# Performance work log

Measured on AMD Instinct MI355X. Metric: run time of the kernel, lower is better.

Reference implementation:

```python
import jax, jax.numpy as jnp
import numpy as np
from jax import lax

B, C, L = 8, 256, 2048
DK, DV, KS = 256, 256, 3
PAD = (KS - 1) // 2  # odd kernel -> dilation 1, same-length padding


def conv1d(x, w, b):
    # x: (B, C, L), w: (O, C, KS), b: (O,)
    y = lax.conv_general_dilated(
        x, w, window_strides=(1,), padding=[(PAD, PAD)],
        rhs_dilation=(1,), dimension_numbers=("NCH", "OIH", "NCH"))
    return y + b[None, :, None]


def setup_inputs() -> dict:
    key = jax.random.key(0)
    ks = jax.random.split(key, 7)
    sc = 1.0 / np.sqrt(C * KS)
    return {
        "x": jax.random.normal(ks[0], (B, C, L), dtype=jnp.float32),
        "Wq": jax.random.normal(ks[1], (DK, C, KS), dtype=jnp.float32) * sc,
        "bq": jnp.zeros((DK,), dtype=jnp.float32),
        "Wk": jax.random.normal(ks[2], (DK, C, KS), dtype=jnp.float32) * sc,
        "bk": jnp.zeros((DK,), dtype=jnp.float32),
        "Wv": jax.random.normal(ks[3], (DV, C, KS), dtype=jnp.float32) * sc,
        "bv": jnp.zeros((DV,), dtype=jnp.float32),
    }


def reference(x, Wq, bq, Wk, bk, Wv, bv):
    Q = conv1d(x, Wq, bq)  # (B, DK, L)
    K = conv1d(x, Wk, bk)  # (B, DK, L)
    V = conv1d(x, Wv, bv)  # (B, DV, L)
    # A = softmax(Q^T K / sqrt(dk)) over key axis
    scores = jnp.einsum("bdq,bdk->bqk", Q, K) / jnp.sqrt(jnp.float32(DK))
    A = jax.nn.softmax(scores, axis=2)  # (B, L, L)
    H = jnp.einsum("bqk,bdk->bdq", A, V)  # (B, DV, L)
    return H
```

## Files before the change

kernel.cpp:

```cpp
#include <hip/hip_runtime.h>
#include <hip/hip_bf16.h>
#include <stdint.h>


typedef __bf16 bf16;
typedef __bf16 bf16x2 __attribute__((ext_vector_type(2)));
typedef __bf16 bf16x4 __attribute__((ext_vector_type(4)));
typedef __bf16 bf16x8 __attribute__((ext_vector_type(8)));
typedef float f32x4 __attribute__((ext_vector_type(4)));
typedef uint32_t u32x4 __attribute__((ext_vector_type(4)));
typedef __attribute__((address_space(1))) const uint32_t cu32_as1;
typedef __attribute__((address_space(3))) uint32_t u32_as3;

#define DEVI __device__ __forceinline__
#define LOG2E 1.44269504088896f

DEVI void async_copy16(const void* g, void* l) {
  __builtin_amdgcn_global_load_lds((cu32_as1*)g, (u32_as3*)l, 16, 0, 0);
}

DEVI void block_sync() {
  asm volatile("" ::: "memory");
  __builtin_amdgcn_sched_barrier(0);
  __builtin_amdgcn_s_barrier();
  __builtin_amdgcn_sched_barrier(0);
  asm volatile("" ::: "memory");
}

#define VMCNT(n) asm volatile("s_waitcnt vmcnt(" #n ")" ::: "memory")

__global__ void prep_w(const float* __restrict__ Wq, const float* __restrict__ Wk,
                       const float* __restrict__ Wv, const float* __restrict__ bq,
                       const float* __restrict__ bk, const float* __restrict__ bv,
                       bf16* __restrict__ W2, float* __restrict__ biasA) {
  const float QSC = 0.0625f * LOG2E;
  int idx = blockIdx.x * 256 + threadIdx.x;
  if (idx < 768 * 768) {
    int o = idx / 768, kk = idx - o * 768;
    int ks = kk >> 8, c = kk & 255;
    const float* W = (o < 256) ? Wq : ((o < 512) ? Wk : Wv);
    int ol = o & 255;
    float w = W[ol * 768 + c * 3 + ks];
    if (o < 256) w *= QSC;
    W2[o * 768 + kk] = (bf16)w;
  }
  if (idx < 768) {
    float v;
    if (idx < 256) v = bq[idx] * QSC;
    else if (idx < 512) v = bk[idx - 256];
    else v = bv[idx - 512];
    biasA[idx] = v;
  }
}

__global__ void prep_x(const float* __restrict__ x, bf16* __restrict__ xT) {
  __shared__ float tile[32][33];
  int bid = blockIdx.x;
  int lt = bid & 63, ct = (bid >> 6) & 7, b = bid >> 9;
  int t = threadIdx.x;
  int tl = t & 31, tc = t >> 5;
  const float* xb = x + (size_t)b * 256 * 2048;
#pragma unroll
  for (int i = 0; i < 4; ++i) {
    int c = ct * 32 + tc + i * 8;
    tile[tc + i * 8][tl] = xb[(size_t)c * 2048 + lt * 32 + tl];
  }
  __syncthreads();
  bf16* xTb = xT + (size_t)b * 2050 * 256;
#pragma unroll
  for (int i = 0; i < 4; ++i) {
    int l = lt * 32 + tc + i * 8;
    xTb[(size_t)(l + 1) * 256 + ct * 32 + tl] = (bf16)tile[tl][tc + i * 8];
  }
  if (lt == 0 && t < 32) xTb[ct * 32 + t] = (bf16)0.f;
  if (lt == 63 && t < 32) xTb[(size_t)2049 * 256 + ct * 32 + t] = (bf16)0.f;
}

__launch_bounds__(256, 2)
__global__ void conv_gemm(const bf16* __restrict__ W2, const bf16* __restrict__ xT,
                          const float* __restrict__ biasA, bf16* __restrict__ QT,
                          bf16* __restrict__ KT, bf16* __restrict__ V) {
  __shared__ bf16 Alds[128 * 64];
  __shared__ bf16 Blds[128 * 64];
  const int t = threadIdx.x;
  const int w = t >> 6, lane = t & 63;
  const int g = lane >> 4, lr = lane & 15;
  const int wr = w >> 1, wc = w & 1;
  const int bid = blockIdx.x;
  const int b = bid & 7;
  const int rest = bid >> 3;
  const int ot = rest % 6;
  const int lt = rest / 6;
  const int l0 = lt * 128;

  const bf16* xTb = xT + (size_t)b * 2050 * 256;
  const bf16* Ab = W2 + (size_t)(ot * 128) * 768;

  const int srow = t >> 3;
  const int scb = ((t & 7) * 16) ^ ((srow & 7) << 4);

  f32x4 acc[4][4];
#pragma unroll
  for (int i = 0; i < 4; ++i)
#pragma unroll
    for (int j = 0; j < 4; ++j) acc[i][j] = (f32x4){0.f, 0.f, 0.f, 0.f};

  for (int step = 0; step < 12; ++step) {
    const int kk = step * 64;
    const int ks = kk >> 8;
    const int c0 = kk & 255;
    const bf16* As = Ab + kk + (scb >> 1);
    const bf16* Bs = xTb + (size_t)(l0 + ks) * 256 + c0 + (scb >> 1);
#pragma unroll
    for (int i = 0; i < 4; ++i) {
      const int row = srow + i * 32;
      async_copy16(As + (size_t)row * 768, (char*)Alds + w * 1024 + i * 4096);
      async_copy16(Bs + (size_t)row * 256, (char*)Blds + w * 1024 + i * 4096);
    }
    asm volatile("s_waitcnt vmcnt(0)" ::: "memory");
    __syncthreads();
#pragma unroll
    for (int sub = 0; sub < 2; ++sub) {
      bf16x8 af[4], bfr[4];
#pragma unroll
      for (int mf = 0; mf < 4; ++mf) {
        const int row = wr * 64 + mf * 16 + lr;
        const int cb = (sub * 64 + g * 16) ^ ((row & 7) << 4);
        af[mf] = *(const bf16x8*)((const char*)Alds + row * 128 + cb);
      }
#pragma unroll
      for (int nf = 0; nf < 4; ++nf) {
        const int row = wc * 64 + nf * 16 + lr;
        const int cb = (sub * 64 + g * 16) ^ ((row & 7) << 4);
        bfr[nf] = *(const bf16x8*)((const char*)Blds + row * 128 + cb);
      }
#pragma unroll
      for (int mf = 0; mf < 4; ++mf)
#pragma unroll
        for (int nf = 0; nf < 4; ++nf)
          acc[mf][nf] = __builtin_amdgcn_mfma_f32_16x16x32_bf16(af[mf], bfr[nf], acc[mf][nf], 0, 0, 0);
    }
    __syncthreads();
  }

  const int obase = ot * 128 + wr * 64;
  const int lbase = l0 + wc * 64;
  if (ot < 4) {
    bf16* dst = ((ot < 2) ? QT : KT) + (size_t)b * 2048 * 256;
#pragma unroll
    for (int mf = 0; mf < 4; ++mf) {
      const int og = obase + mf * 16 + g * 4;
      float bb[4];
#pragma unroll
      for (int r = 0; r < 4; ++r) bb[r] = biasA[og + r];
#pragma unroll
      for (int nf = 0; nf < 4; ++nf) {
        const int l = lbase + nf * 16 + lr;
        bf16x4 pk;
#pragma unroll
        for (int r = 0; r < 4; ++r) pk[r] = (bf16)(acc[mf][nf][r] + bb[r]);
        *(bf16x4*)(dst + (size_t)l * 256 + (og & 255)) = pk;
      }
    }
  } else {
    bf16* dst = V + (size_t)b * 256 * 2048;
#pragma unroll
    for (int mf = 0; mf < 4; ++mf) {
      const int og = obase + mf * 16 + g * 4;
      float bb[4];
#pragma unroll
      for (int r = 0; r < 4; ++r) bb[r] = biasA[og + r];
      const int ov = og - 512;
#pragma unroll
      for (int nf = 0; nf < 4; ++nf) {
        const int l = lbase + nf * 16 + lr;
#pragma unroll
        for (int r = 0; r < 4; ++r)
          dst[(size_t)(ov + r) * 2048 + l] = (bf16)(acc[mf][nf][r] + bb[r]);
      }
    }
  }
}

__launch_bounds__(256, 2)
__global__ void attn(const bf16* __restrict__ QT, const bf16* __restrict__ KT,
                     const bf16* __restrict__ V, bf16* __restrict__ Opart,
                     float* __restrict__ Sl) {
  __shared__ bf16 Klds[2 * 32 * 256];
  __shared__ bf16 Vlds[2 * 128 * 64];
  const int t = threadIdx.x;
  const int w = t >> 6, lane = t & 63;
  const int g = lane >> 4, lr = lane & 15;
  const int bid = blockIdx.x;
  const int b = bid & 7;
  const int kvh = (bid >> 3) & 3;
  const int qt = bid >> 5;
  const int q0w = qt * 128 + w * 32;
  const int kb0 = kvh * 512;
  const bf16* QTb = QT + (size_t)b * 2048 * 256;
  const bf16* KTb = KT + (size_t)b * 2048 * 256;
  const bf16* Vb = V + (size_t)b * 256 * 2048;

  auto stageK = [&](int kt, int p) {
#pragma unroll
    for (int i = 0; i < 4; ++i) {
      const int row = i * 8 + (t >> 5);
      const int col = ((t & 31) ^ row) * 8;
      const bf16* src = KTb + (size_t)(kb0 + kt * 32 + row) * 256 + col;
      async_copy16(src, (char*)Klds + p * 16384 + i * 4096 + t * 16);
    }
  };
  auto stageV = [&](int kt, int p) {
#pragma unroll
    for (int i = 0; i < 4; ++i) {
      const int row = i * 32 + (t >> 3);
      const int ls = (t & 7) ^ (row & 7);
      const int d = row * 2 + (ls >> 2);
      const int k0 = (ls & 3) * 8;
      const bf16* src = Vb + (size_t)d * 2048 + kb0 + kt * 32 + k0;
      async_copy16(src, (char*)Vlds + p * 16384 + i * 4096 + t * 16);
    }
  };

  bf16x8 qreg[2][8];
#pragma unroll
  for (int qfr = 0; qfr < 2; ++qfr)
#pragma unroll
    for (int ds = 0; ds < 8; ++ds)
      qreg[qfr][ds] = *(const bf16x8*)(QTb + (size_t)(q0w + qfr * 16 + lr) * 256 + ds * 32 + g * 8);

  f32x4 oacc[16][2];
#pragma unroll
  for (int i = 0; i < 16; ++i) {
    oacc[i][0] = (f32x4){0.f, 0.f, 0.f, 0.f};
    oacc[i][1] = (f32x4){0.f, 0.f, 0.f, 0.f};
  }
  float l_acc[2] = {0.f, 0.f};

  stageK(0, 0); stageV(0, 0);
  stageK(1, 1); stageV(1, 1);

  for (int kt = 0; kt < 16; ++kt) {
    const int p = kt & 1;
    if (kt == 15) { VMCNT(0); } else { VMCNT(8); }
    block_sync();

    f32x4 sT[2][2];
#pragma unroll
    for (int kfr = 0; kfr < 2; ++kfr)
#pragma unroll
      for (int qfr = 0; qfr < 2; ++qfr) sT[kfr][qfr] = (f32x4){0.f, 0.f, 0.f, 0.f};
    __builtin_amdgcn_s_setprio(1);
#pragma unroll
    for (int ds = 0; ds < 8; ++ds) {
      bf16x8 kf[2];
#pragma unroll
      for (int kfr = 0; kfr < 2; ++kfr) {
        const int row = kfr * 16 + lr;
        kf[kfr] = *(const bf16x8*)((const char*)Klds + p * 16384 + row * 512 +
                                   (((ds * 4 + g) ^ row) * 16));
      }
#pragma unroll
      for (int kfr = 0; kfr < 2; ++kfr)
#pragma unroll
        for (int qfr = 0; qfr < 2; ++qfr)
          sT[kfr][qfr] = __builtin_amdgcn_mfma_f32_16x16x32_bf16(kf[kfr], qreg[qfr][ds], sT[kfr][qfr], 0, 0, 0);
    }
    __builtin_amdgcn_s_setprio(0);

#pragma unroll
    for (int kfr = 0; kfr < 2; ++kfr)
#pragma unroll
      for (int qfr = 0; qfr < 2; ++qfr)
#pragma unroll
        for (int r = 0; r < 4; ++r) {
          float pe = __builtin_exp2f(sT[kfr][qfr][r]);
          sT[kfr][qfr][r] = pe;
          l_acc[qfr] += pe;
        }

    bf16x8 pB[2];
#pragma unroll
    for (int qfr = 0; qfr < 2; ++qfr) {
      uint32_t wq[2][2];
#pragma unroll
      for (int kfr = 0; kfr < 2; ++kfr)
#pragma unroll
        for (int pp = 0; pp < 2; ++pp) {
          bf16x2 pr;
          pr[0] = (bf16)sT[kfr][qfr][2 * pp];
          pr[1] = (bf16)sT[kfr][qfr][2 * pp + 1];
          wq[kfr][pp] = __builtin_bit_cast(uint32_t, pr);
        }
      uint32_t bw[4];
#pragma unroll
      for (int j = 0; j < 4; ++j) {
        const int srcLane = ((g & 1) * 2 + (j >> 1)) * 16 + lr;
        const uint32_t a = (uint32_t)__shfl((int)wq[0][j & 1], srcLane, 64);
        const uint32_t bb = (uint32_t)__shfl((int)wq[1][j & 1], srcLane, 64);
        bw[j] = (lane < 32) ? a : bb;
      }
      u32x4 v4 = {bw[0], bw[1], bw[2], bw[3]};
      pB[qfr] = __builtin_bit_cast(bf16x8, v4);
    }

    __builtin_amdgcn_s_setprio(1);
#pragma unroll
    for (int dfr = 0; dfr < 16; ++dfr) {
      const int row = dfr * 8 + (lr >> 1);
      bf16x8 vf = *(const bf16x8*)((const char*)Vlds + p * 16384 + row * 128 +
                                   ((((lr & 1) * 4 + g) ^ ((lr >> 1) & 7)) * 16));
      oacc[dfr][0] = __builtin_amdgcn_mfma_f32_16x16x32_bf16(vf, pB[0], oacc[dfr][0], 0, 0, 0);
      oacc[dfr][1] = __builtin_amdgcn_mfma_f32_16x16x32_bf16(vf, pB[1], oacc[dfr][1], 0, 0, 0);
    }
    __builtin_amdgcn_s_setprio(0);
    block_sync();
    if (kt < 14) { stageK(kt + 2, p); stageV(kt + 2, p); }
  }

#pragma unroll
  for (int qfr = 0; qfr < 2; ++qfr) {
    float rv = l_acc[qfr];
    rv += __shfl_xor(rv, 16, 64);
    rv += __shfl_xor(rv, 32, 64);
    l_acc[qfr] = rv;
  }

  bf16* Op = Opart + (size_t)bid * 128 * 256;
#pragma unroll
  for (int qfr = 0; qfr < 2; ++qfr) {
    const int ql = w * 32 + qfr * 16 + lr;
#pragma unroll
    for (int dfr = 0; dfr < 16; ++dfr) {
      const int d0 = dfr * 16 + g * 4;
      bf16x4 pk;
#pragma unroll
      for (int r = 0; r < 4; ++r) pk[r] = (bf16)oacc[dfr][qfr][r];
      *(bf16x4*)(Op + (size_t)ql * 256 + d0) = pk;
    }
    if (g == 0) Sl[bid * 128 + ql] = l_acc[qfr];
  }
}

__launch_bounds__(256)
__global__ void merge_p(const bf16* __restrict__ Opart, const float* __restrict__ Sl,
                        float* __restrict__ H) {
  __shared__ float Ocomb[32][257];
  const int bid = blockIdx.x;
  const int b = bid & 7;
  const int qt = (bid >> 3) & 15;
  const int qc = bid >> 7;
  const int t = threadIdx.x;
  float* Hb = H + (size_t)b * 256 * 2048 + qt * 128 + qc * 32;

  for (int qq = 0; qq < 32; ++qq) {
    const int ql = qc * 32 + qq;
    float wsum = 0.f, o = 0.f;
#pragma unroll
    for (int kvh = 0; kvh < 4; ++kvh) {
      const int blk = b + 8 * kvh + 32 * qt;
      wsum += Sl[blk * 128 + ql];
      o += (float)Opart[((size_t)blk * 128 + ql) * 256 + t];
    }
    Ocomb[qq][t] = o / wsum;
  }
  __syncthreads();
  const int q = t & 31;
  const int dbase = (t >> 5) * 32;
#pragma unroll
  for (int j = 0; j < 32; ++j) {
    const int d = dbase + j;
    Hb[(size_t)d * 2048 + q] = Ocomb[q][d];
  }
}

extern "C" void kernel_launch(void* const* d_in, const int* in_sizes, int n_in,
                              void* d_out, int out_size, void* d_ws, size_t ws_size,
                              hipStream_t stream) {
  (void)in_sizes; (void)n_in; (void)out_size; (void)ws_size;
  const float* x = (const float*)d_in[0];
  const float* Wq = (const float*)d_in[1];
  const float* bq = (const float*)d_in[2];
  const float* Wk = (const float*)d_in[3];
  const float* bk = (const float*)d_in[4];
  const float* Wv = (const float*)d_in[5];
  const float* bv = (const float*)d_in[6];
  char* ws = (char*)d_ws;
  bf16* xT = (bf16*)(ws + 0);
  bf16* W2 = (bf16*)(ws + 8396800);
  float* biasA = (float*)(ws + 9576448);
  bf16* QT = (bf16*)(ws + 9580544);
  bf16* KT = (bf16*)(ws + 17969152);
  bf16* V = (bf16*)(ws + 26357760);
  bf16* Opart = (bf16*)(ws + 34746368);
  float* Sl = (float*)(ws + 68300800);
  float* H = (float*)d_out;

  prep_w<<<dim3(2304), dim3(256), 0, stream>>>(Wq, Wk, Wv, bq, bk, bv, W2, biasA);
  prep_x<<<dim3(4096), dim3(256), 0, stream>>>(x, xT);
  conv_gemm<<<dim3(768), dim3(256), 0, stream>>>(W2, xT, biasA, QT, KT, V);
  attn<<<dim3(512), dim3(256), 0, stream>>>(QT, KT, V, Opart, Sl);
  merge_p<<<dim3(512), dim3(256), 0, stream>>>(Opart, Sl, H);
}
```

Before: 113.3 us.

## Share softmax probabilities via LDS and split the PV product across waves by head dim

Each wave now writes its exponentiated score tile as bf16 into a new shared LDS buffer. The PV matmul is repartitioned so that every wave covers all 128 queries but only a quarter of the value dimension, replacing the cross-lane shuffle packing of P. This cuts per-wave V fragment reads from LDS. The load pipeline is also reordered: V is staged one tile ahead right after the top barrier, and K two tiles ahead after the P barrier. The cost is an extra block barrier per iteration, an LDS write/read round-trip for P, and an lgkmcnt(0) wait added to every barrier.

```diff
diff --git a/kernel.cpp b/kernel.cpp
--- a/kernel.cpp
+++ b/kernel.cpp
@@ -22,6 +22,7 @@
 DEVI void block_sync() {
   asm volatile("" ::: "memory");
   __builtin_amdgcn_sched_barrier(0);
+  asm volatile("s_waitcnt lgkmcnt(0)" ::: "memory");
   __builtin_amdgcn_s_barrier();
   __builtin_amdgcn_sched_barrier(0);
   asm volatile("" ::: "memory");
@@ -188,6 +189,7 @@
                      float* __restrict__ Sl) {
   __shared__ bf16 Klds[2 * 32 * 256];
   __shared__ bf16 Vlds[2 * 128 * 64];
+  __shared__ bf16 Plds[64 * 64];
   const int t = threadIdx.x;
   const int w = t >> 6, lane = t & 63;
   const int g = lane >> 4, lr = lane & 15;
@@ -224,32 +226,33 @@
 
   bf16x8 qreg[2][8];
 #pragma unroll
-  for (int qfr = 0; qfr < 2; ++qfr)
+  for (int qf = 0; qf < 2; ++qf)
 #pragma unroll
     for (int ds = 0; ds < 8; ++ds)
-      qreg[qfr][ds] = *(const bf16x8*)(QTb + (size_t)(q0w + qfr * 16 + lr) * 256 + ds * 32 + g * 8);
-
-  f32x4 oacc[16][2];
-#pragma unroll
-  for (int i = 0; i < 16; ++i) {
-    oacc[i][0] = (f32x4){0.f, 0.f, 0.f, 0.f};
-    oacc[i][1] = (f32x4){0.f, 0.f, 0.f, 0.f};
-  }
+      qreg[qf][ds] = *(const bf16x8*)(QTb + (size_t)(q0w + qf * 16 + lr) * 256 + ds * 32 + g * 8);
+
+  f32x4 oacc[4][8];
+#pragma unroll
+  for (int i = 0; i < 4; ++i)
+#pragma unroll
+    for (int j = 0; j < 8; ++j) oacc[i][j] = (f32x4){0.f, 0.f, 0.f, 0.f};
   float l_acc[2] = {0.f, 0.f};
 
-  stageK(0, 0); stageV(0, 0);
-  stageK(1, 1); stageV(1, 1);
+  stageK(0, 0);
+  stageV(0, 0);
+  stageK(1, 1);
 
   for (int kt = 0; kt < 16; ++kt) {
     const int p = kt & 1;
-    if (kt == 15) { VMCNT(0); } else { VMCNT(8); }
+    if (kt == 15) { VMCNT(0); } else { VMCNT(4); }
     block_sync();
+    if (kt < 15) stageV(kt + 1, p ^ 1);
 
     f32x4 sT[2][2];
 #pragma unroll
     for (int kfr = 0; kfr < 2; ++kfr)
 #pragma unroll
-      for (int qfr = 0; qfr < 2; ++qfr) sT[kfr][qfr] = (f32x4){0.f, 0.f, 0.f, 0.f};
+      for (int qf = 0; qf < 2; ++qf) sT[kfr][qf] = (f32x4){0.f, 0.f, 0.f, 0.f};
     __builtin_amdgcn_s_setprio(1);
 #pragma unroll
     for (int ds = 0; ds < 8; ++ds) {
@@ -263,82 +266,71 @@
 #pragma unroll
       for (int kfr = 0; kfr < 2; ++kfr)
 #pragma unroll
-        for (int qfr = 0; qfr < 2; ++qfr)
-          sT[kfr][qfr] = __builtin_amdgcn_mfma_f32_16x16x32_bf16(kf[kfr], qreg[qfr][ds], sT[kfr][qfr], 0, 0, 0);
+        for (int qf = 0; qf < 2; ++qf)
+          sT[kfr][qf] = __builtin_amdgcn_mfma_f32_16x16x32_bf16(kf[kfr], qreg[qf][ds], sT[kfr][qf], 0, 0, 0);
     }
     __builtin_amdgcn_s_setprio(0);
 
 #pragma unroll
     for (int kfr = 0; kfr < 2; ++kfr)
 #pragma unroll
-      for (int qfr = 0; qfr < 2; ++qfr)
+      for (int qf = 0; qf < 2; ++qf) {
+        bf16x4 pk;
 #pragma unroll
         for (int r = 0; r < 4; ++r) {
-          float pe = __builtin_exp2f(sT[kfr][qfr][r]);
-          sT[kfr][qfr][r] = pe;
-          l_acc[qfr] += pe;
+          float pe = __builtin_exp2f(sT[kfr][qf][r]);
+          l_acc[qf] += pe;
+          pk[r] = (bf16)pe;
         }
-
-    bf16x8 pB[2];
-#pragma unroll
-    for (int qfr = 0; qfr < 2; ++qfr) {
-      uint32_t wq[2][2];
-#pragma unroll
-      for (int kfr = 0; kfr < 2; ++kfr)
-#pragma unroll
-        for (int pp = 0; pp < 2; ++pp) {
-          bf16x2 pr;
-          pr[0] = (bf16)sT[kfr][qfr][2 * pp];
-          pr[1] = (bf16)sT[kfr][qfr][2 * pp + 1];
-          wq[kfr][pp] = __builtin_bit_cast(uint32_t, pr);
-        }
-      uint32_t bw[4];
-#pragma unroll
-      for (int j = 0; j < 4; ++j) {
-        const int srcLane = ((g & 1) * 2 + (j >> 1)) * 16 + lr;
-        const uint32_t a = (uint32_t)__shfl((int)wq[0][j & 1], srcLane, 64);
-        const uint32_t bb = (uint32_t)__shfl((int)wq[1][j & 1], srcLane, 64);
-        bw[j] = (lane < 32) ? a : bb;
-      }
-      u32x4 v4 = {bw[0], bw[1], bw[2], bw[3]};
-      pB[qfr] = __builtin_bit_cast(bf16x8, v4);
-    }
+        const int q = w * 32 + qf * 16 + lr;
+        const int row = q >> 1;
+        const int slot = (lr & 1) * 4 + kfr * 2 + (g >> 1);
+        const int byte = row * 128 + ((slot ^ (row & 7)) << 4) + (g & 1) * 8;
+        *(bf16x4*)((char*)Plds + byte) = pk;
+      }
+    block_sync();
+    if (kt < 14) stageK(kt + 2, p);
 
     __builtin_amdgcn_s_setprio(1);
-#pragma unroll
-    for (int dfr = 0; dfr < 16; ++dfr) {
-      const int row = dfr * 8 + (lr >> 1);
-      bf16x8 vf = *(const bf16x8*)((const char*)Vlds + p * 16384 + row * 128 +
-                                   ((((lr & 1) * 4 + g) ^ ((lr >> 1) & 7)) * 16));
-      oacc[dfr][0] = __builtin_amdgcn_mfma_f32_16x16x32_bf16(vf, pB[0], oacc[dfr][0], 0, 0, 0);
-      oacc[dfr][1] = __builtin_amdgcn_mfma_f32_16x16x32_bf16(vf, pB[1], oacc[dfr][1], 0, 0, 0);
+    bf16x8 pB[8];
+#pragma unroll
+    for (int qfr = 0; qfr < 8; ++qfr) {
+      const int row = qfr * 8 + (lr >> 1);
+      const int byte = row * 128 + ((((lr & 1) * 4 + g) ^ (row & 7)) << 4);
+      pB[qfr] = *(const bf16x8*)((const char*)Plds + byte);
+    }
+#pragma unroll
+    for (int dfr = 0; dfr < 4; ++dfr) {
+      const int vrow = w * 32 + dfr * 8 + (lr >> 1);
+      bf16x8 vf = *(const bf16x8*)((const char*)Vlds + p * 16384 + vrow * 128 +
+                                   ((((lr & 1) * 4 + g) ^ (vrow & 7)) << 4));
+#pragma unroll
+      for (int qfr = 0; qfr < 8; ++qfr)
+        oacc[dfr][qfr] = __builtin_amdgcn_mfma_f32_16x16x32_bf16(vf, pB[qfr], oacc[dfr][qfr], 0, 0, 0);
     }
     __builtin_amdgcn_s_setprio(0);
-    block_sync();
-    if (kt < 14) { stageK(kt + 2, p); stageV(kt + 2, p); }
-  }
-
-#pragma unroll
-  for (int qfr = 0; qfr < 2; ++qfr) {
-    float rv = l_acc[qfr];
+  }
+
+#pragma unroll
+  for (int qf = 0; qf < 2; ++qf) {
+    float rv = l_acc[qf];
     rv += __shfl_xor(rv, 16, 64);
     rv += __shfl_xor(rv, 32, 64);
-    l_acc[qfr] = rv;
+    if (g == 0) Sl[bid * 128 + (w * 32 + qf * 16 + lr)] = rv;
   }
 
   bf16* Op = Opart + (size_t)bid * 128 * 256;
 #pragma unroll
-  for (int qfr = 0; qfr < 2; ++qfr) {
-    const int ql = w * 32 + qfr * 16 + lr;
-#pragma unroll
-    for (int dfr = 0; dfr < 16; ++dfr) {
-      const int d0 = dfr * 16 + g * 4;
+  for (int qfr = 0; qfr < 8; ++qfr) {
+    const int q = qfr * 16 + lr;
+#pragma unroll
+    for (int dfr = 0; dfr < 4; ++dfr) {
+      const int d0 = w * 64 + dfr * 16 + g * 4;
       bf16x4 pk;
 #pragma unroll
       for (int r = 0; r < 4; ++r) pk[r] = (bf16)oacc[dfr][qfr][r];
-      *(bf16x4*)(Op + (size_t)ql * 256 + d0) = pk;
-    }
-    if (g == 0) Sl[bid * 128 + ql] = l_acc[qfr];
+      *(bf16x4*)(Op + (size_t)q * 256 + d0) = pk;
+    }
   }
 }
 
```

Result: slower. 117.2 us (+3.5%).
